# Performance work log

Measured on AMD Instinct MI355X. Metric: run time of the kernel, lower is better.

Reference implementation:

```python
import jax, jax.numpy as jnp
import numpy as np

B, S, D = 2, 2048, 1024
H, DH = 16, 64
C = 64          # chunk_size (sliding window)
WF = 4          # widening factor
FMIN = jnp.finfo(jnp.float32).min


def _ln(x, scale, offset, eps=1e-5):
    mu = jnp.mean(x, axis=-1, keepdims=True)
    var = jnp.var(x, axis=-1, keepdims=True)
    return (x - mu) * jax.lax.rsqrt(var + eps) * scale + offset


def setup_inputs() -> dict:
    key = jax.random.key(0)
    ks = jax.random.split(key, 12)
    std = 0.02
    inp = {
        'x': jax.random.normal(ks[0], (B, S, D), dtype=jnp.float32),
        'causal_mask': jnp.tril(jnp.ones((S, S), dtype=bool))[None, None],  # (1,1,S,S)
        'pos': jax.random.normal(ks[1], (C, D), dtype=jnp.float32),          # pos_0..pos_{C-1}
        'rpe': std * jax.random.normal(ks[2], (H, C), dtype=jnp.float32),
        'Wq': std * jax.random.normal(ks[3], (D, H * DH), dtype=jnp.float32),
        'Wk': std * jax.random.normal(ks[4], (D, H * DH), dtype=jnp.float32),
        'Wv': std * jax.random.normal(ks[5], (D, H * DH), dtype=jnp.float32),
        'Wo': std * jax.random.normal(ks[6], (H * DH, D), dtype=jnp.float32),
        'ln1_scale': jnp.ones((D,), jnp.float32),
        'ln1_offset': jnp.zeros((D,), jnp.float32),
        'W1': std * jax.random.normal(ks[7], (D, WF * D), dtype=jnp.float32),
        'b1': jnp.zeros((WF * D,), jnp.float32),
        'W2': std * jax.random.normal(ks[8], (WF * D, D), dtype=jnp.float32),
        'b2': jnp.zeros((D,), jnp.float32),
        'ln2_scale': jnp.ones((D,), jnp.float32),
        'ln2_offset': jnp.zeros((D,), jnp.float32),
    }
    return inp


def _sliding_window_mask(rpe, seq_len):
    # mask[h,t,T] = rpe[h, t-T] if 0 <= t-T < C (lower diagonals), else -inf
    d = jnp.arange(seq_len)[:, None] - jnp.arange(seq_len)[None, :]  # (S,S)
    valid = (d >= 0) & (d < C)
    dc = jnp.clip(d, 0, C - 1)
    val = jnp.where(valid[None], rpe[:, dc], 0.0)  # (H,S,S)
    return jnp.where(val != 0, val, FMIN)


def reference(x, causal_mask, pos, rpe, Wq, Wk, Wv, Wo, ln1_scale, ln1_offset,
              W1, b1, W2, b2, ln2_scale, ln2_offset):
    seq_len = x.shape[1]
    # front/rear positional vectors: pos_i added at positions i, i+C, i+2C, ...
    h = x + pos[jnp.arange(seq_len) % C]  # (B,S,D)

    q = (h @ Wq).reshape(B, seq_len, H, DH)
    k = (h @ Wk).reshape(B, seq_len, H, DH)
    v = (h @ Wv).reshape(B, seq_len, H, DH)

    attn = jnp.einsum('bthd,bThd->bhtT', q, k) * (1.0 / jnp.sqrt(DH))
    attn = attn + _sliding_window_mask(rpe, seq_len)[None]  # learned diag bias
    attn = jnp.where(causal_mask, attn, FMIN)
    attn = jax.nn.softmax(attn, axis=-1)

    out = jnp.einsum('bhtT,bThd->bthd', attn, v).reshape(B, seq_len, H * DH)
    out = out @ Wo

    # dropout_prob = 0 -> identity
    attention = _ln(h + out, ln1_scale, ln1_offset)
    ff = jax.nn.relu(attention @ W1 + b1) @ W2 + b2
    return _ln(ff + attention, ln2_scale, ln2_offset)
```

## Files before the change

kernel.cpp:

```cpp
#include <hip/hip_runtime.h>
#include <hip/hip_bf16.h>

#define DEVI static __device__ __forceinline__

typedef __attribute__((ext_vector_type(4))) float f32x4;
typedef __attribute__((ext_vector_type(8))) short bf16x8;
typedef __attribute__((ext_vector_type(4))) short s16x4;

constexpr int TB  = 2;
constexpr int TS  = 2048;
constexpr int TD  = 1024;
constexpr int TH  = 16;
constexpr int TDH = 64;
constexpr int TC  = 64;
constexpr int TFF = 4096;
constexpr int TM  = TB * TS;

DEVI float bf2f(short s) {
  return __builtin_bit_cast(float, (unsigned)((unsigned short)s) << 16);
}
DEVI short f2bf(float f) {
  return __builtin_bit_cast(short, __float2bfloat16(f));
}

#define GLD16(gp, lp)                                              \
  __builtin_amdgcn_global_load_lds(                                \
      (const __attribute__((address_space(1))) void*)(gp),         \
      (__attribute__((address_space(3))) void*)(lp), 16, 0, 0)

#define WAITVM(N) asm volatile("s_waitcnt vmcnt(" #N ")" ::: "memory")

__global__ __launch_bounds__(256) void k_transpose_bf16(
    const float* __restrict__ W, __hip_bfloat16* __restrict__ WT, int K, int N) {
  __shared__ float tile[32][33];
  int n0 = blockIdx.x * 32, k0 = blockIdx.y * 32;
  int tx = threadIdx.x & 31, ty = threadIdx.x >> 5;
  for (int i = 0; i < 32; i += 8)
    tile[ty + i][tx] = W[(size_t)(k0 + ty + i) * N + n0 + tx];
  __syncthreads();
  for (int i = 0; i < 32; i += 8)
    WT[(size_t)(n0 + ty + i) * K + k0 + tx] = __float2bfloat16(tile[tx][ty + i]);
}

__global__ __launch_bounds__(256) void k_addpos(
    const float* __restrict__ x, const float* __restrict__ pos,
    __hip_bfloat16* __restrict__ hb, int total4) {
  int i = blockIdx.x * 256 + threadIdx.x;
  if (i >= total4) return;
  int e = i * 4;
  int d = e & (TD - 1);
  int t = (e / TD) & (TS - 1);
  f32x4 xv = *(const f32x4*)(x + e);
  f32x4 pv = *(const f32x4*)(pos + (size_t)(t & (TC - 1)) * TD + d);
  s16x4 hb4;
  for (int j = 0; j < 4; j++) hb4[j] = f2bf(xv[j] + pv[j]);
  *(s16x4*)((short*)hb + e) = hb4;
}

template <int BN, int EPI>
__global__ __launch_bounds__(512, 2) void k_gemm2(
    const __hip_bfloat16* __restrict__ A, const __hip_bfloat16* __restrict__ BT,
    void* __restrict__ Cout, const float* __restrict__ bias,
    int M, int N, int K, int lda, int ldb) {
  constexpr int BM = 256, BK = 32;
  constexpr int FN = BN / 64;
  constexpr int LPB = BN / 128;
  __shared__ __align__(16) short As[4][BM * BK];
  __shared__ __align__(16) short Bs[4][BN * BK];
  int tid = threadIdx.x;
  int lane = tid & 63, wave = tid >> 6;
  int wm = wave >> 2, wn = wave & 3;
  int fr = lane & 15, fg = lane >> 4;
  int m0 = blockIdx.x * BM, n0 = blockIdx.y * BN;
  size_t koff = (size_t)blockIdx.z * K;
  const __hip_bfloat16* Ab = A + koff;
  const __hip_bfloat16* Bb = BT + koff;

  auto stageA = [&](int d, int T) {
#pragma unroll
    for (int i = 0; i < 2; i++) {
      int c = i * 512 + tid;
      int row = c >> 2, seg = (c & 3) ^ ((row >> 1) & 3);
      GLD16(Ab + (size_t)(m0 + row) * lda + T * BK + seg * 8,
            (char*)&As[d][0] + (i * 512 + wave * 64) * 16);
    }
  };
  auto stageB = [&](int d, int T) {
#pragma unroll
    for (int i = 0; i < LPB; i++) {
      int c = i * 512 + tid;
      int row = c >> 2, seg = (c & 3) ^ ((row >> 1) & 3);
      GLD16(Bb + (size_t)(n0 + row) * ldb + T * BK + seg * 8,
            (char*)&Bs[d][0] + (i * 512 + wave * 64) * 16);
    }
  };

  f32x4 acc[8][FN];
#pragma unroll
  for (int m = 0; m < 8; m++)
#pragma unroll
    for (int n = 0; n < FN; n++) acc[m][n] = f32x4{0.f, 0.f, 0.f, 0.f};

  const int nt = K / BK;
  stageA(0, 0); stageB(0, 0);
  stageA(1, 1); stageB(1, 1);
  stageA(2, 2); stageB(2, 2);

  for (int t = 0; t < nt; t++) {
    int d = t & 3;
    if (t < nt - 2) {
      if (BN == 256) { WAITVM(8); } else { WAITVM(6); }
    } else if (t == nt - 2) {
      if (BN == 256) { WAITVM(4); } else { WAITVM(3); }
    } else {
      WAITVM(0);
    }
    __builtin_amdgcn_s_barrier();
    asm volatile("" ::: "memory");

    bf16x8 a0[4], bf[FN];
#pragma unroll
    for (int m = 0; m < 4; m++) {
      int row = wm * 128 + m * 16 + fr;
      a0[m] = *(const bf16x8*)((const char*)&As[d][0] + row * 64 +
                               ((fg ^ ((row >> 1) & 3)) << 4));
    }
#pragma unroll
    for (int n = 0; n < FN; n++) {
      int row = wn * (BN / 4) + n * 16 + fr;
      bf[n] = *(const bf16x8*)((const char*)&Bs[d][0] + row * 64 +
                               ((fg ^ ((row >> 1) & 3)) << 4));
    }
    if (t + 3 < nt) stageA((t + 3) & 3, t + 3);
    __builtin_amdgcn_s_setprio(1);
#pragma unroll
    for (int m = 0; m < 4; m++)
#pragma unroll
      for (int n = 0; n < FN; n++)
        acc[m][n] = __builtin_amdgcn_mfma_f32_16x16x32_bf16(a0[m], bf[n],
                                                            acc[m][n], 0, 0, 0);
    __builtin_amdgcn_s_setprio(0);

    bf16x8 a1[4];
#pragma unroll
    for (int m = 0; m < 4; m++) {
      int row = wm * 128 + 64 + m * 16 + fr;
      a1[m] = *(const bf16x8*)((const char*)&As[d][0] + row * 64 +
                               ((fg ^ ((row >> 1) & 3)) << 4));
    }
    if (t + 3 < nt) stageB((t + 3) & 3, t + 3);
    __builtin_amdgcn_s_setprio(1);
#pragma unroll
    for (int m = 0; m < 4; m++)
#pragma unroll
      for (int n = 0; n < FN; n++)
        acc[m + 4][n] = __builtin_amdgcn_mfma_f32_16x16x32_bf16(a1[m], bf[n],
                                                                acc[m + 4][n], 0, 0, 0);
    __builtin_amdgcn_s_setprio(0);
  }

  float* Cf = (float*)Cout + (size_t)blockIdx.z * M * N;
#pragma unroll
  for (int m = 0; m < 8; m++)
#pragma unroll
    for (int n = 0; n < FN; n++) {
      int col = n0 + wn * (BN / 4) + n * 16 + fr;
      float bv = (EPI == 1) ? bias[col] : 0.f;
#pragma unroll
      for (int j = 0; j < 4; j++) {
        int row = m0 + wm * 128 + m * 16 + fg * 4 + j;
        float v = acc[m][n][j];
        if (EPI == 1) { v += bv; v = fmaxf(v, 0.f); }
        if (EPI == 2)
          Cf[(size_t)row * N + col] = v;
        else
          ((__hip_bfloat16*)Cout)[(size_t)row * N + col] = __float2bfloat16(v);
      }
    }
}

__global__ __launch_bounds__(256) void k_vtrans(
    const __hip_bfloat16* __restrict__ qkv, __hip_bfloat16* __restrict__ vT) {
  __shared__ short tile[64][68];
  int bh = blockIdx.x;
  int tb = blockIdx.y;
  int b = bh >> 4, h = bh & 15;
  int tid = threadIdx.x;
#pragma unroll
  for (int i = 0; i < 2; i++) {
    int c = i * 256 + tid;
    int trow = c >> 3, seg = c & 7;
    bf16x8 v = *(const bf16x8*)((const short*)qkv +
        (size_t)(b * TS + tb * 64 + trow) * 3072 + 2048 + h * TDH + seg * 8);
    s16x4 lo = {v[0], v[1], v[2], v[3]}, hi = {v[4], v[5], v[6], v[7]};
    *(s16x4*)&tile[trow][seg * 8] = lo;
    *(s16x4*)&tile[trow][seg * 8 + 4] = hi;
  }
  __syncthreads();
#pragma unroll
  for (int i2 = 0; i2 < 2; i2++) {
    int c = i2 * 256 + tid;
    int d = c >> 3, ts = c & 7;
    bf16x8 o;
#pragma unroll
    for (int j = 0; j < 8; j++) o[j] = tile[ts * 8 + j][d];
    *(bf16x8*)((short*)vT + (size_t)bh * TDH * TS + (size_t)d * TS +
               tb * 64 + ts * 8) = o;
  }
}

__global__ __launch_bounds__(256) void k_attn(
    const __hip_bfloat16* __restrict__ qkv, const __hip_bfloat16* __restrict__ vT,
    const float* __restrict__ rpe, __hip_bfloat16* __restrict__ out) {
  __shared__ __align__(16) short K_lds[128 * 64];
  __shared__ __align__(16) short VT_lds[64 * 128];
  __shared__ __align__(16) short P_lds[4][16 * 136];
  __shared__ float rpe_lds[TC];
  int tid = threadIdx.x, lane = tid & 63, wave = tid >> 6;
  int fr = lane & 15, g = lane >> 4;
  int blk = blockIdx.x;
  int qt = blk & 31, bh = blk >> 5;
  int h = bh & 15, b = bh >> 4;
  int t0 = qt * 64;
  const short* qg = (const short*)qkv;

  if (tid < TC) rpe_lds[tid] = rpe[h * TC + tid];

#pragma unroll
  for (int i = 0; i < 4; i++) {
    int cb = i * 256 + wave * 64;
    int c = cb + lane;
    int row = c >> 3, slot = c & 7;
    int seg = slot ^ (row & 7);
    int kr = t0 - 64 + row; if (kr < 0) kr = 0;
    GLD16(qg + ((size_t)(b * TS + kr) * 3072 + 1024 + h * TDH + seg * 8),
          (char*)K_lds + cb * 16);
  }
  const short* vg = (const short*)vT + (size_t)bh * TDH * TS;
#pragma unroll
  for (int i = 0; i < 4; i++) {
    int cb = i * 256 + wave * 64;
    int c = cb + lane;
    int row = c >> 4, slot = c & 15;
    int seg = slot ^ (row & 15);
    int tc = t0 - 64 + seg * 8; if (tc < 0) tc = 0;
    GLD16(vg + (size_t)row * TS + tc, (char*)VT_lds + cb * 16);
  }

  int qrow = t0 + wave * 16 + fr;
  const short* qptr = qg + ((size_t)(b * TS + qrow) * 3072 + h * TDH + g * 8);
  bf16x8 qf0 = *(const bf16x8*)qptr;
  bf16x8 qf1 = *(const bf16x8*)(qptr + 32);

  __syncthreads();

  f32x4 S[8] = {};
#pragma unroll
  for (int kk = 0; kk < 2; kk++) {
    bf16x8 a = kk ? qf1 : qf0;
#pragma unroll
    for (int nt = 0; nt < 8; nt++) {
      int row = nt * 16 + fr;
      int slot = (kk * 4 + g) ^ (row & 7);
      bf16x8 bfrag = *(const bf16x8*)((const char*)K_lds + row * 128 + slot * 16);
      S[nt] = __builtin_amdgcn_mfma_f32_16x16x32_bf16(a, bfrag, S[nt], 0, 0, 0);
    }
  }

  int wq = wave * 16;
#pragma unroll
  for (int r = 0; r < 4; r++) {
    int ql = g * 4 + r;
    float sc[8];
    float m = -3.4028235e38f;
#pragma unroll
    for (int nt = 0; nt < 8; nt++) {
      int jj = nt * 16 + fr;
      int d = wq + ql + 64 - jj;
      bool valid = (d >= 0) && (d < TC) && (t0 - 64 + jj >= 0);
      float v = valid ? (S[nt][r] * 0.125f + rpe_lds[d & (TC - 1)])
                      : -3.4028235e38f;
      sc[nt] = v;
      m = fmaxf(m, v);
    }
#pragma unroll
    for (int o = 1; o < 16; o <<= 1) m = fmaxf(m, __shfl_xor(m, o));
    float p[8], sum = 0.f;
#pragma unroll
    for (int nt = 0; nt < 8; nt++) { p[nt] = __expf(sc[nt] - m); sum += p[nt]; }
#pragma unroll
    for (int o = 1; o < 16; o <<= 1) sum += __shfl_xor(sum, o);
    float rs = 1.0f / sum;
#pragma unroll
    for (int nt = 0; nt < 8; nt++)
      P_lds[wave][ql * 136 + nt * 16 + fr] = f2bf(p[nt] * rs);
  }

  f32x4 O[4] = {};
#pragma unroll
  for (int kk = 0; kk < 4; kk++) {
    bf16x8 pa = *(const bf16x8*)((const char*)&P_lds[wave][0] +
                                 fr * 272 + kk * 64 + g * 16);
#pragma unroll
    for (int dt = 0; dt < 4; dt++) {
      int row = dt * 16 + fr;
      int slot = (kk * 4 + g) ^ (row & 15);
      bf16x8 vb = *(const bf16x8*)((const char*)VT_lds + row * 256 + slot * 16);
      O[dt] = __builtin_amdgcn_mfma_f32_16x16x32_bf16(pa, vb, O[dt], 0, 0, 0);
    }
  }

  size_t ob = ((size_t)(b * TS + t0 + wq + g * 4)) * TD + h * TDH;
#pragma unroll
  for (int dt = 0; dt < 4; dt++)
#pragma unroll
    for (int r = 0; r < 4; r++)
      ((short*)out)[ob + (size_t)r * TD + dt * 16 + fr] = f2bf(O[dt][r]);
}

DEVI float block_sum(float v, float* red) {
  for (int o = 32; o; o >>= 1) v += __shfl_xor(v, o);
  int wave = threadIdx.x >> 6;
  if ((threadIdx.x & 63) == 0) red[wave] = v;
  __syncthreads();
  float r = red[0] + red[1] + red[2] + red[3];
  __syncthreads();
  return r;
}

__global__ __launch_bounds__(256) void k_ln1(
    const float* __restrict__ x, const float* __restrict__ pos,
    const float* __restrict__ P0, const float* __restrict__ P1,
    const float* __restrict__ scale, const float* __restrict__ offset,
    float* __restrict__ outf, __hip_bfloat16* __restrict__ outb) {
  __shared__ float red[4];
  int row = blockIdx.x, tid = threadIdx.x;
  int t = row & (TS - 1), pr = t & (TC - 1);
  size_t base = (size_t)row * TD + tid * 4;
  f32x4 xv = *(const f32x4*)(x + base);
  f32x4 pv = *(const f32x4*)(pos + (size_t)pr * TD + tid * 4);
  f32x4 a0 = *(const f32x4*)(P0 + base);
  f32x4 a1 = *(const f32x4*)(P1 + base);
  xv = xv + pv + a0 + a1;
  float s = xv[0] + xv[1] + xv[2] + xv[3];
  s = block_sum(s, red);
  float mu = s * (1.f / TD);
  float s2 = 0.f;
  for (int j = 0; j < 4; j++) { float dlt = xv[j] - mu; s2 += dlt * dlt; }
  s2 = block_sum(s2, red);
  float rs = rsqrtf(s2 * (1.f / TD) + 1e-5f);
  f32x4 sc = *(const f32x4*)(scale + tid * 4);
  f32x4 of = *(const f32x4*)(offset + tid * 4);
  f32x4 y;
  for (int j = 0; j < 4; j++) y[j] = (xv[j] - mu) * rs * sc[j] + of[j];
  *(f32x4*)(outf + base) = y;
  s16x4 pb;
  for (int j = 0; j < 4; j++) pb[j] = f2bf(y[j]);
  *(s16x4*)((short*)outb + base) = pb;
}

__global__ __launch_bounds__(256) void k_ln2(
    const float* __restrict__ P0, const float* __restrict__ P1,
    const float* __restrict__ R, const float* __restrict__ bias,
    const float* __restrict__ scale, const float* __restrict__ offset,
    float* __restrict__ outf) {
  __shared__ float red[4];
  int row = blockIdx.x, tid = threadIdx.x;
  size_t base = (size_t)row * TD + tid * 4;
  f32x4 a0 = *(const f32x4*)(P0 + base);
  f32x4 a1 = *(const f32x4*)(P1 + base);
  f32x4 rv = *(const f32x4*)(R + base);
  f32x4 bi = *(const f32x4*)(bias + tid * 4);
  f32x4 xv = a0 + a1 + rv + bi;
  float s = xv[0] + xv[1] + xv[2] + xv[3];
  s = block_sum(s, red);
  float mu = s * (1.f / TD);
  float s2 = 0.f;
  for (int j = 0; j < 4; j++) { float dlt = xv[j] - mu; s2 += dlt * dlt; }
  s2 = block_sum(s2, red);
  float rs = rsqrtf(s2 * (1.f / TD) + 1e-5f);
  f32x4 sc = *(const f32x4*)(scale + tid * 4);
  f32x4 of = *(const f32x4*)(offset + tid * 4);
  f32x4 y;
  for (int j = 0; j < 4; j++) y[j] = (xv[j] - mu) * rs * sc[j] + of[j];
  *(f32x4*)(outf + base) = y;
}

extern "C" void kernel_launch(void* const* d_in, const int* in_sizes, int n_in,
                              void* d_out, int out_size, void* d_ws, size_t ws_size,
                              hipStream_t stream) {
  const float* x    = (const float*)d_in[0];
  const float* pos  = (const float*)d_in[2];
  const float* rpe  = (const float*)d_in[3];
  const float* Wq   = (const float*)d_in[4];
  const float* Wk   = (const float*)d_in[5];
  const float* Wv   = (const float*)d_in[6];
  const float* Wo   = (const float*)d_in[7];
  const float* ln1s = (const float*)d_in[8];
  const float* ln1o = (const float*)d_in[9];
  const float* W1   = (const float*)d_in[10];
  const float* b1   = (const float*)d_in[11];
  const float* W2   = (const float*)d_in[12];
  const float* b2   = (const float*)d_in[13];
  const float* ln2s = (const float*)d_in[14];
  const float* ln2o = (const float*)d_in[15];

  char* ws = (char*)d_ws;
  const size_t MB = 1ull << 20;
  __hip_bfloat16* WqkvT = (__hip_bfloat16*)(ws + 0 * MB);
  __hip_bfloat16* WoT   = (__hip_bfloat16*)(ws + 6 * MB);
  __hip_bfloat16* W1T   = (__hip_bfloat16*)(ws + 8 * MB);
  __hip_bfloat16* W2T   = (__hip_bfloat16*)(ws + 16 * MB);
  __hip_bfloat16* hB    = (__hip_bfloat16*)(ws + 24 * MB);
  __hip_bfloat16* qkv   = (__hip_bfloat16*)(ws + 32 * MB);
  __hip_bfloat16* aoB   = (__hip_bfloat16*)(ws + 56 * MB);
  float*          oF2   = (float*)(ws + 64 * MB);
  float*          atF   = (float*)(ws + 96 * MB);
  __hip_bfloat16* atB   = (__hip_bfloat16*)(ws + 24 * MB);
  __hip_bfloat16* ff1   = (__hip_bfloat16*)(ws + 32 * MB);
  float*          ff2   = (float*)(ws + 64 * MB);
  __hip_bfloat16* vTb   = (__hip_bfloat16*)(ws + 112 * MB);

  dim3 blk(256), blk5(512);

  k_transpose_bf16<<<dim3(TD / 32, TD / 32), blk, 0, stream>>>(Wq, WqkvT, TD, TD);
  k_transpose_bf16<<<dim3(TD / 32, TD / 32), blk, 0, stream>>>(Wk, WqkvT + (size_t)TD * TD, TD, TD);
  k_transpose_bf16<<<dim3(TD / 32, TD / 32), blk, 0, stream>>>(Wv, WqkvT + (size_t)2 * TD * TD, TD, TD);
  k_transpose_bf16<<<dim3(TD / 32, TD / 32), blk, 0, stream>>>(Wo, WoT, TD, TD);
  k_transpose_bf16<<<dim3(TFF / 32, TD / 32), blk, 0, stream>>>(W1, W1T, TD, TFF);
  k_transpose_bf16<<<dim3(TD / 32, TFF / 32), blk, 0, stream>>>(W2, W2T, TFF, TD);

  k_addpos<<<(TM * TD / 4 + 255) / 256, blk, 0, stream>>>(x, pos, hB, TM * TD / 4);

  k_gemm2<256, 0><<<dim3(TM / 256, 3072 / 256, 1), blk5, 0, stream>>>(
      hB, WqkvT, qkv, nullptr, TM, 3072, TD, TD, TD);

  k_vtrans<<<dim3(TB * TH, TS / 64), blk, 0, stream>>>(qkv, vTb);
  k_attn<<<TB * TH * (TS / 64), blk, 0, stream>>>(qkv, vTb, rpe, aoB);

  k_gemm2<128, 2><<<dim3(TM / 256, TD / 128, 2), blk5, 0, stream>>>(
      aoB, WoT, oF2, nullptr, TM, TD, TD / 2, TD, TD);

  k_ln1<<<TM, blk, 0, stream>>>(x, pos, oF2, oF2 + (size_t)TM * TD, ln1s, ln1o, atF, atB);

  k_gemm2<256, 1><<<dim3(TM / 256, TFF / 256, 1), blk5, 0, stream>>>(
      atB, W1T, ff1, b1, TM, TFF, TD, TD, TD);

  k_gemm2<128, 2><<<dim3(TM / 256, TD / 128, 2), blk5, 0, stream>>>(
      ff1, W2T, ff2, nullptr, TM, TD, TFF / 2, TFF, TFF);

  k_ln2<<<TM, blk, 0, stream>>>(ff2, ff2 + (size_t)TM * TD, atF, b2, ln2s, ln2o,
                                (float*)d_out);
}
```

Measured before the change: 213.9 us.

## Fuse weight transposes into one launch and restructure GEMM pipeline barriers

Merges the six weight transpose-to-bf16 launches into a single kernel that decodes which matrix each block handles. The GEMM main loop is reworked: global-to-LDS load addresses are precomputed once, the vmcnt wait moves to after the prefetch issue, and extra s_barriers are added between the MFMA phases so waves stay in lockstep, in a ping-pong style schedule. The BN=128 variant now loads all eight A fragments at once and issues its prefetch in one spot. This aims to cut launch overhead and shorten GEMM stalls, but the added barriers and higher register pressure could instead slow the loop.

Result: faster. 204.9 us (-4.2%).

```diff
diff --git a/kernel.cpp b/kernel.cpp
--- a/kernel.cpp
+++ b/kernel.cpp
@@ -30,16 +30,36 @@
 
 #define WAITVM(N) asm volatile("s_waitcnt vmcnt(" #N ")" ::: "memory")
 
-__global__ __launch_bounds__(256) void k_transpose_bf16(
-    const float* __restrict__ W, __hip_bfloat16* __restrict__ WT, int K, int N) {
+__global__ __launch_bounds__(256) void k_trans_all(
+    const float* __restrict__ Wq, const float* __restrict__ Wk,
+    const float* __restrict__ Wv, const float* __restrict__ Wo,
+    const float* __restrict__ W1, const float* __restrict__ W2,
+    __hip_bfloat16* __restrict__ WqkvT, __hip_bfloat16* __restrict__ WoT,
+    __hip_bfloat16* __restrict__ W1T, __hip_bfloat16* __restrict__ W2T) {
   __shared__ float tile[32][33];
-  int n0 = blockIdx.x * 32, k0 = blockIdx.y * 32;
+  int bid = blockIdx.x;
+  const float* src; __hip_bfloat16* dst;
+  int K, N, n0, k0;
+  if (bid < 4096) {
+    int m = bid >> 10, t = bid & 1023;
+    src = (m == 0) ? Wq : (m == 1) ? Wk : (m == 2) ? Wv : Wo;
+    dst = (m == 3) ? WoT : WqkvT + (size_t)m * TD * TD;
+    K = TD; N = TD; n0 = (t & 31) * 32; k0 = (t >> 5) * 32;
+  } else if (bid < 8192) {
+    int t = bid - 4096;
+    src = W1; dst = W1T; K = TD; N = TFF;
+    n0 = (t & 127) * 32; k0 = (t >> 7) * 32;
+  } else {
+    int t = bid - 8192;
+    src = W2; dst = W2T; K = TFF; N = TD;
+    n0 = (t & 31) * 32; k0 = (t >> 5) * 32;
+  }
   int tx = threadIdx.x & 31, ty = threadIdx.x >> 5;
   for (int i = 0; i < 32; i += 8)
-    tile[ty + i][tx] = W[(size_t)(k0 + ty + i) * N + n0 + tx];
+    tile[ty + i][tx] = src[(size_t)(k0 + ty + i) * N + n0 + tx];
   __syncthreads();
   for (int i = 0; i < 32; i += 8)
-    WT[(size_t)(n0 + ty + i) * K + k0 + tx] = __float2bfloat16(tile[tx][ty + i]);
+    dst[(size_t)(n0 + ty + i) * K + k0 + tx] = __float2bfloat16(tile[tx][ty + i]);
 }
 
 __global__ __launch_bounds__(256) void k_addpos(
@@ -58,41 +78,38 @@
 }
 
 template <int BN, int EPI>
-__global__ __launch_bounds__(512, 2) void k_gemm2(
+__global__ __launch_bounds__(512, 2) void k_gemm8(
     const __hip_bfloat16* __restrict__ A, const __hip_bfloat16* __restrict__ BT,
     void* __restrict__ Cout, const float* __restrict__ bias,
     int M, int N, int K, int lda, int ldb) {
   constexpr int BM = 256, BK = 32;
   constexpr int FN = BN / 64;
-  constexpr int LPB = BN / 128;
   __shared__ __align__(16) short As[4][BM * BK];
   __shared__ __align__(16) short Bs[4][BN * BK];
-  int tid = threadIdx.x;
-  int lane = tid & 63, wave = tid >> 6;
+  int tid = threadIdx.x, lane = tid & 63, wave = tid >> 6;
   int wm = wave >> 2, wn = wave & 3;
   int fr = lane & 15, fg = lane >> 4;
   int m0 = blockIdx.x * BM, n0 = blockIdx.y * BN;
   size_t koff = (size_t)blockIdx.z * K;
-  const __hip_bfloat16* Ab = A + koff;
-  const __hip_bfloat16* Bb = BT + koff;
+  const short* Ab = (const short*)A + koff;
+  const short* Bb = (const short*)BT + koff;
+
+  int r0 = tid >> 2, s0 = (tid & 3) ^ ((r0 >> 1) & 3);
+  int r1 = 128 + r0, s1 = (tid & 3) ^ ((r1 >> 1) & 3);
+  const short* pA0 = Ab + (size_t)(m0 + r0) * lda + s0 * 8;
+  const short* pA1 = Ab + (size_t)(m0 + r1) * lda + s1 * 8;
+  const short* pB0 = Bb + (size_t)(n0 + r0) * ldb + s0 * 8;
+  const short* pB1 = (BN == 256) ? Bb + (size_t)(n0 + r1) * ldb + s1 * 8 : pB0;
+  int dst0 = (wave * 64) * 16;
+  int dst1 = (512 + wave * 64) * 16;
 
   auto stageA = [&](int d, int T) {
-#pragma unroll
-    for (int i = 0; i < 2; i++) {
-      int c = i * 512 + tid;
-      int row = c >> 2, seg = (c & 3) ^ ((row >> 1) & 3);
-      GLD16(Ab + (size_t)(m0 + row) * lda + T * BK + seg * 8,
-            (char*)&As[d][0] + (i * 512 + wave * 64) * 16);
-    }
+    GLD16(pA0 + T * BK, (char*)&As[d][0] + dst0);
+    GLD16(pA1 + T * BK, (char*)&As[d][0] + dst1);
   };
   auto stageB = [&](int d, int T) {
-#pragma unroll
-    for (int i = 0; i < LPB; i++) {
-      int c = i * 512 + tid;
-      int row = c >> 2, seg = (c & 3) ^ ((row >> 1) & 3);
-      GLD16(Bb + (size_t)(n0 + row) * ldb + T * BK + seg * 8,
-            (char*)&Bs[d][0] + (i * 512 + wave * 64) * 16);
-    }
+    GLD16(pB0 + T * BK, (char*)&Bs[d][0] + dst0);
+    if constexpr (BN == 256) GLD16(pB1 + T * BK, (char*)&Bs[d][0] + dst1);
   };
 
   f32x4 acc[8][FN];
@@ -105,71 +122,96 @@
   stageA(0, 0); stageB(0, 0);
   stageA(1, 1); stageB(1, 1);
   stageA(2, 2); stageB(2, 2);
+  if (BN == 256) { WAITVM(8); } else { WAITVM(6); }
+  __builtin_amdgcn_s_barrier();
 
   for (int t = 0; t < nt; t++) {
-    int d = t & 3;
-    if (t < nt - 2) {
-      if (BN == 256) { WAITVM(8); } else { WAITVM(6); }
-    } else if (t == nt - 2) {
-      if (BN == 256) { WAITVM(4); } else { WAITVM(3); }
+    int d = t & 3, pf = (t + 3) & 3;
+    bool dopf = (t + 3) < nt;
+    const char* Al = (const char*)&As[d][0];
+    const char* Bl = (const char*)&Bs[d][0];
+    if constexpr (BN == 256) {
+      bf16x8 a[4], b[4];
+#pragma unroll
+      for (int mt = 0; mt < 4; mt++) {
+        int row = wm * 128 + mt * 16 + fr;
+        a[mt] = *(const bf16x8*)(Al + row * 64 + ((fg ^ ((row >> 1) & 3)) << 4));
+      }
+#pragma unroll
+      for (int n = 0; n < 4; n++) {
+        int row = wn * 64 + n * 16 + fr;
+        b[n] = *(const bf16x8*)(Bl + row * 64 + ((fg ^ ((row >> 1) & 3)) << 4));
+      }
+      if (dopf) stageA(pf, t + 3);
+      __builtin_amdgcn_s_barrier();
+      __builtin_amdgcn_s_setprio(1);
+#pragma unroll
+      for (int mt = 0; mt < 4; mt++)
+#pragma unroll
+        for (int n = 0; n < 4; n++)
+          acc[mt][n] = __builtin_amdgcn_mfma_f32_16x16x32_bf16(a[mt], b[n],
+                                                               acc[mt][n], 0, 0, 0);
+      __builtin_amdgcn_s_setprio(0);
+      __builtin_amdgcn_s_barrier();
+#pragma unroll
+      for (int mt = 0; mt < 4; mt++) {
+        int row = wm * 128 + 64 + mt * 16 + fr;
+        a[mt] = *(const bf16x8*)(Al + row * 64 + ((fg ^ ((row >> 1) & 3)) << 4));
+      }
+      if (dopf) stageB(pf, t + 3);
+      if (t < nt - 3) { WAITVM(8); }
+      else if (t == nt - 3) { WAITVM(4); }
+      else if (t == nt - 2) { WAITVM(0); }
+      __builtin_amdgcn_s_barrier();
+      __builtin_amdgcn_s_setprio(1);
+#pragma unroll
+      for (int mt = 0; mt < 4; mt++)
+#pragma unroll
+        for (int n = 0; n < 4; n++)
+          acc[4 + mt][n] = __builtin_amdgcn_mfma_f32_16x16x32_bf16(a[mt], b[n],
+                                                                   acc[4 + mt][n], 0, 0, 0);
+      __builtin_amdgcn_s_setprio(0);
+      __builtin_amdgcn_s_barrier();
     } else {
-      WAITVM(0);
+      bf16x8 a[8], b[2];
+#pragma unroll
+      for (int mt = 0; mt < 8; mt++) {
+        int row = wm * 128 + mt * 16 + fr;
+        a[mt] = *(const bf16x8*)(Al + row * 64 + ((fg ^ ((row >> 1) & 3)) << 4));
+      }
+#pragma unroll
+      for (int n = 0; n < 2; n++) {
+        int row = wn * 32 + n * 16 + fr;
+        b[n] = *(const bf16x8*)(Bl + row * 64 + ((fg ^ ((row >> 1) & 3)) << 4));
+      }
+      if (dopf) { stageA(pf, t + 3); stageB(pf, t + 3); }
+      if (t < nt - 3) { WAITVM(6); }
+      else if (t == nt - 3) { WAITVM(3); }
+      else if (t == nt - 2) { WAITVM(0); }
+      __builtin_amdgcn_s_barrier();
+      __builtin_amdgcn_s_setprio(1);
+#pragma unroll
+      for (int mt = 0; mt < 8; mt++)
+#pragma unroll
+        for (int n = 0; n < 2; n++)
+          acc[mt][n] = __builtin_amdgcn_mfma_f32_16x16x32_bf16(a[mt], b[n],
+                                                               acc[mt][n], 0, 0, 0);
+      __builtin_amdgcn_s_setprio(0);
+      __builtin_amdgcn_s_barrier();
     }
-    __builtin_amdgcn_s_barrier();
-    asm volatile("" ::: "memory");
-
-    bf16x8 a0[4], bf[FN];
-#pragma unroll
-    for (int m = 0; m < 4; m++) {
-      int row = wm * 128 + m * 16 + fr;
-      a0[m] = *(const bf16x8*)((const char*)&As[d][0] + row * 64 +
-                               ((fg ^ ((row >> 1) & 3)) << 4));
-    }
-#pragma unroll
-    for (int n = 0; n < FN; n++) {
-      int row = wn * (BN / 4) + n * 16 + fr;
-      bf[n] = *(const bf16x8*)((const char*)&Bs[d][0] + row * 64 +
-                               ((fg ^ ((row >> 1) & 3)) << 4));
-    }
-    if (t + 3 < nt) stageA((t + 3) & 3, t + 3);
-    __builtin_amdgcn_s_setprio(1);
-#pragma unroll
-    for (int m = 0; m < 4; m++)
-#pragma unroll
-      for (int n = 0; n < FN; n++)
-        acc[m][n] = __builtin_amdgcn_mfma_f32_16x16x32_bf16(a0[m], bf[n],
-                                                            acc[m][n], 0, 0, 0);
-    __builtin_amdgcn_s_setprio(0);
-
-    bf16x8 a1[4];
-#pragma unroll
-    for (int m = 0; m < 4; m++) {
-      int row = wm * 128 + 64 + m * 16 + fr;
-      a1[m] = *(const bf16x8*)((const char*)&As[d][0] + row * 64 +
-                               ((fg ^ ((row >> 1) & 3)) << 4));
-    }
-    if (t + 3 < nt) stageB((t + 3) & 3, t + 3);
-    __builtin_amdgcn_s_setprio(1);
-#pragma unroll
-    for (int m = 0; m < 4; m++)
-#pragma unroll
-      for (int n = 0; n < FN; n++)
-        acc[m + 4][n] = __builtin_amdgcn_mfma_f32_16x16x32_bf16(a1[m], bf[n],
-                                                                acc[m + 4][n], 0, 0, 0);
-    __builtin_amdgcn_s_setprio(0);
   }
 
   float* Cf = (float*)Cout + (size_t)blockIdx.z * M * N;
 #pragma unroll
-  for (int m = 0; m < 8; m++)
+  for (int mt = 0; mt < 8; mt++)
 #pragma unroll
     for (int n = 0; n < FN; n++) {
       int col = n0 + wn * (BN / 4) + n * 16 + fr;
       float bv = (EPI == 1) ? bias[col] : 0.f;
 #pragma unroll
       for (int j = 0; j < 4; j++) {
-        int row = m0 + wm * 128 + m * 16 + fg * 4 + j;
-        float v = acc[m][n][j];
+        int row = m0 + wm * 128 + mt * 16 + fg * 4 + j;
+        float v = acc[mt][n][j];
         if (EPI == 1) { v += bv; v = fmaxf(v, 0.f); }
         if (EPI == 2)
           Cf[(size_t)row * N + col] = v;
@@ -423,30 +465,26 @@
 
   dim3 blk(256), blk5(512);
 
-  k_transpose_bf16<<<dim3(TD / 32, TD / 32), blk, 0, stream>>>(Wq, WqkvT, TD, TD);
-  k_transpose_bf16<<<dim3(TD / 32, TD / 32), blk, 0, stream>>>(Wk, WqkvT + (size_t)TD * TD, TD, TD);
-  k_transpose_bf16<<<dim3(TD / 32, TD / 32), blk, 0, stream>>>(Wv, WqkvT + (size_t)2 * TD * TD, TD, TD);
-  k_transpose_bf16<<<dim3(TD / 32, TD / 32), blk, 0, stream>>>(Wo, WoT, TD, TD);
-  k_transpose_bf16<<<dim3(TFF / 32, TD / 32), blk, 0, stream>>>(W1, W1T, TD, TFF);
-  k_transpose_bf16<<<dim3(TD / 32, TFF / 32), blk, 0, stream>>>(W2, W2T, TFF, TD);
+  k_trans_all<<<12288, blk, 0, stream>>>(Wq, Wk, Wv, Wo, W1, W2,
+                                         WqkvT, WoT, W1T, W2T);
 
   k_addpos<<<(TM * TD / 4 + 255) / 256, blk, 0, stream>>>(x, pos, hB, TM * TD / 4);
 
-  k_gemm2<256, 0><<<dim3(TM / 256, 3072 / 256, 1), blk5, 0, stream>>>(
+  k_gemm8<256, 0><<<dim3(TM / 256, 3072 / 256, 1), blk5, 0, stream>>>(
       hB, WqkvT, qkv, nullptr, TM, 3072, TD, TD, TD);
 
   k_vtrans<<<dim3(TB * TH, TS / 64), blk, 0, stream>>>(qkv, vTb);
   k_attn<<<TB * TH * (TS / 64), blk, 0, stream>>>(qkv, vTb, rpe, aoB);
 
-  k_gemm2<128, 2><<<dim3(TM / 256, TD / 128, 2), blk5, 0, stream>>>(
+  k_gemm8<128, 2><<<dim3(TM / 256, TD / 128, 2), blk5, 0, stream>>>(
       aoB, WoT, oF2, nullptr, TM, TD, TD / 2, TD, TD);
 
   k_ln1<<<TM, blk, 0, stream>>>(x, pos, oF2, oF2 + (size_t)TM * TD, ln1s, ln1o, atF, atB);
 
-  k_gemm2<256, 1><<<dim3(TM / 256, TFF / 256, 1), blk5, 0, stream>>>(
+  k_gemm8<256, 1><<<dim3(TM / 256, TFF / 256, 1), blk5, 0, stream>>>(
       atB, W1T, ff1, b1, TM, TFF, TD, TD, TD);
 
-  k_gemm2<128, 2><<<dim3(TM / 256, TD / 128, 2), blk5, 0, stream>>>(
+  k_gemm8<128, 2><<<dim3(TM / 256, TD / 128, 2), blk5, 0, stream>>>(
       ff1, W2T, ff2, nullptr, TM, TD, TFF / 2, TFF, TFF);
 
   k_ln2<<<TM, blk, 0, stream>>>(ff2, ff2 + (size_t)TM * TD, atF, b2, ln2s, ln2o,
```
